# Performance work log

Hardware: AMD Instinct MI355X
Metric: run time of the kernel (lower is better)

Reference implementation:

```python
import jax, jax.numpy as jnp
import numpy as np

B, N, D, NS, HID = 256, 1024, 64, 8, 128
ITERS, SINK_ITERS, MESH_ITERS = 3, 8, 4
MESH_LR = 3.0
EPS = 1e-8


def _grid():
    # build_coords with latent_resolution=(32,32): meshgrid('xy'), flattened to [1024,2]
    x = np.linspace(0.0, 1.0, 32)
    xv, yv = np.meshgrid(x, x)
    g = np.stack([xv.reshape(-1), yv.reshape(-1)], axis=-1)
    return jnp.asarray(g, dtype=jnp.float32)


def layer_norm(x, g, b):
    m = jnp.mean(x, axis=-1, keepdims=True)
    v = jnp.var(x, axis=-1, keepdims=True)
    return (x - m) * jax.lax.rsqrt(v + 1e-5) * g + b


def cdist(k, q):
    # Euclidean pairwise distance: k [b,n,d], q [b,s,d] -> [b,n,s]
    d2 = (jnp.sum(k * k, -1)[..., :, None] + jnp.sum(q * q, -1)[..., None, :]
          - 2.0 * jnp.einsum('bnd,bsd->bns', k, q))
    return jnp.sqrt(jnp.maximum(d2, 1e-12))


def sinkhorn(C, a, b, u=None, v=None, n_iters=SINK_ITERS):
    # log-domain Sinkhorn; C [b,n,s], row marginal a [b,n], col marginal b [b,s]
    log_a = jnp.log(a + EPS)
    log_b = jnp.log(b + EPS)
    if u is None:
        u = jnp.zeros_like(a)
    if v is None:
        v = jnp.zeros_like(b)
    K = -C

    def body(carry, _):
        u, v = carry
        u = log_a - jax.scipy.special.logsumexp(K + v[..., None, :], axis=-1)
        v = log_b - jax.scipy.special.logsumexp(K + u[..., :, None], axis=-2)
        return (u, v), None

    (u, v), _ = jax.lax.scan(body, (u, v), None, length=n_iters)
    P = jnp.exp(K + u[..., :, None] + v[..., None, :])
    return P, u, v


def minimize_entropy_of_sinkhorn(C0, a, b, mesh_lr=MESH_LR, n_mesh_iters=MESH_ITERS):
    # MESH: gradient descent on the cost matrix to minimize Sinkhorn plan entropy
    def ent(C):
        P, u, v = sinkhorn(C, a, b)
        H = -jnp.sum(P * jnp.log(P + EPS))
        return H, (u, v)

    C = C0
    u = v = None
    for _ in range(n_mesh_iters):
        (_, (u, v)), g = jax.value_and_grad(ent, has_aux=True)(C)
        C = C - mesh_lr * g
    return C, u, v


def gru_cell(x, h, w_ih, w_hh, b_ih, b_hh):
    gi = x @ w_ih.T + b_ih
    gh = h @ w_hh.T + b_hh
    i_r, i_z, i_n = jnp.split(gi, 3, axis=-1)
    h_r, h_z, h_n = jnp.split(gh, 3, axis=-1)
    r = jax.nn.sigmoid(i_r + h_r)
    z = jax.nn.sigmoid(i_z + h_z)
    n = jnp.tanh(i_n + r * h_n)
    return (1.0 - z) * n + z * h


def setup_inputs() -> dict:
    key = jax.random.key(0)
    ks = jax.random.split(key, 16)
    s = D ** -0.5
    inp = {
        'inputs': jax.random.normal(ks[0], (B, N, D), jnp.float32),
        'noise': jax.random.normal(ks[1], (B, NS, D), jnp.float32),
        'slots_mu': jax.random.normal(ks[2], (1, 1, D), jnp.float32),
        'slots_sigma': jax.random.uniform(ks[3], (1, 1, D), jnp.float32),
        'Wq': jax.random.normal(ks[4], (D, D), jnp.float32) * s,
        'Wk': jax.random.normal(ks[5], (D, D), jnp.float32) * s,
        'Wv': jax.random.normal(ks[6], (D, D), jnp.float32) * s,
        'gru_w_ih': jax.random.normal(ks[7], (3 * D, D), jnp.float32) * s,
        'gru_w_hh': jax.random.normal(ks[8], (3 * D, D), jnp.float32) * s,
        'gru_b_ih': jnp.zeros((3 * D,), jnp.float32),
        'gru_b_hh': jnp.zeros((3 * D,), jnp.float32),
        'fc1_w': jax.random.normal(ks[9], (HID, D), jnp.float32) * s,
        'fc1_b': jnp.zeros((HID,), jnp.float32),
        'fc2_w': jax.random.normal(ks[10], (D, HID), jnp.float32) * (HID ** -0.5),
        'fc2_b': jnp.zeros((D,), jnp.float32),
        'ln_in_g': jnp.ones((D,), jnp.float32), 'ln_in_b': jnp.zeros((D,), jnp.float32),
        'ln_slots_g': jnp.ones((D,), jnp.float32), 'ln_slots_b': jnp.zeros((D,), jnp.float32),
        'ln_ff_g': jnp.ones((D,), jnp.float32), 'ln_ff_b': jnp.zeros((D,), jnp.float32),
        'wi_w': jax.random.normal(ks[11], (1, D), jnp.float32) * s,
        'wi_b': jnp.zeros((1,), jnp.float32),
        'ws_w': jax.random.normal(ks[12], (1, D), jnp.float32) * s,
        'ws_b': jnp.zeros((1,), jnp.float32),
    }
    return inp


def _forward(inputs, noise, slots_mu, slots_sigma, Wq, Wk, Wv,
             gru_w_ih, gru_w_hh, gru_b_ih, gru_b_hh,
             fc1_w, fc1_b, fc2_w, fc2_b,
             ln_in_g, ln_in_b, ln_slots_g, ln_slots_b, ln_ff_g, ln_ff_b,
             wi_w, wi_b, ws_w, ws_b):
    b_s, n, d = inputs.shape
    n_s = NS
    # slots ~ Normal(mu, |sigma|+eps) via reparameterized noise
    slots = slots_mu + (jnp.abs(slots_sigma) + EPS) * noise  # [b, n_s, d]

    x = layer_norm(inputs, ln_in_g, ln_in_b)
    k = x @ Wk.T
    v = x @ Wv.T
    grid = _grid()  # [N, 2]
    a = jax.nn.softmax((x @ wi_w.T + wi_b)[..., 0], axis=-1) * n_s  # [b, n]

    for _ in range(ITERS):
        slots_prev = slots
        s_n = layer_norm(slots, ln_slots_g, ln_slots_b)
        bm = jax.nn.softmax((s_n @ ws_w.T + ws_b)[..., 0], axis=-1) * n_s  # [b, n_s]
        q = s_n @ Wq.T
        C = cdist(k, q)  # [b, n, n_s]
        C, p, qq = minimize_entropy_of_sinkhorn(C, a, bm)
        attn, _, _ = sinkhorn(C, a, bm, u=p, v=qq)
        attn = jnp.transpose(attn, (0, 2, 1))  # [b, n_s, n]
        updates = attn @ v  # [b, n_s, d]
        slot_pos = jnp.einsum('bqk,kd->bqd', attn, grid)  # [b, n_s, 2]
        slots = gru_cell(updates.reshape(b_s * n_s, d),
                         slots_prev.reshape(b_s * n_s, d),
                         gru_w_ih, gru_w_hh, gru_b_ih, gru_b_hh).reshape(b_s, n_s, d)
        slots = slots + (jax.nn.relu(layer_norm(slots, ln_ff_g, ln_ff_b) @ fc1_w.T + fc1_b) @ fc2_w.T + fc2_b)
    return slots, slot_pos.reshape(b_s, n_s, 2), attn


def reference(inputs, noise, slots_mu, slots_sigma, Wq, Wk, Wv,
              gru_w_ih, gru_w_hh, gru_b_ih, gru_b_hh,
              fc1_w, fc1_b, fc2_w, fc2_b,
              ln_in_g, ln_in_b, ln_slots_g, ln_slots_b, ln_ff_g, ln_ff_b,
              wi_w, wi_b, ws_w, ws_b):
    return _forward(inputs, noise, slots_mu, slots_sigma, Wq, Wk, Wv,
                    gru_w_ih, gru_w_hh, gru_b_ih, gru_b_hh,
                    fc1_w, fc1_b, fc2_w, fc2_b,
                    ln_in_g, ln_in_b, ln_slots_g, ln_slots_b, ln_ff_g, ln_ff_b,
                    wi_w, wi_b, ws_w, ws_b)
```

## Files before the change

kernel.cpp:

```cpp
#include <hip/hip_runtime.h>
#include <math.h>

#define NB   256
#define NN   1024
#define ND   64
#define NSL  8
#define NHID 128
#define N_SINK 8
#define N_MESH 4
#define F_LR  3.0f
#define F_EPS 1e-8f

__global__ __launch_bounds__(256) void k_pre(
    const float* __restrict__ inp, const float* __restrict__ Wk,
    const float* __restrict__ lng, const float* __restrict__ lnb,
    const float* __restrict__ wiw, const float* __restrict__ wib,
    float* __restrict__ xout, float* __restrict__ kkout, float* __restrict__ wilog) {
  __shared__ __align__(16) float xs[4][64];
  int wv = threadIdx.x >> 6, ln = threadIdx.x & 63;
  size_t row = (size_t)blockIdx.x * 4 + wv;
  float xi = inp[row * 64 + ln];
  float s1 = xi, s2 = xi * xi;
  #pragma unroll
  for (int m = 32; m >= 1; m >>= 1) { s1 += __shfl_xor(s1, m, 64); s2 += __shfl_xor(s2, m, 64); }
  float mean = s1 * (1.f / 64.f);
  float var  = s2 * (1.f / 64.f) - mean * mean;
  float xn = (xi - mean) * rsqrtf(var + 1e-5f) * lng[ln] + lnb[ln];
  xs[wv][ln] = xn;
  xout[row * 64 + ln] = xn;
  float wl = xn * wiw[ln];
  #pragma unroll
  for (int m = 32; m >= 1; m >>= 1) wl += __shfl_xor(wl, m, 64);
  __syncthreads();
  const float4* w4 = (const float4*)(Wk + ln * 64);
  const float4* x4 = (const float4*)xs[wv];
  float ko = 0.f;
  #pragma unroll
  for (int c = 0; c < 16; ++c) {
    float4 a = w4[c], xv = x4[c];
    ko += a.x * xv.x + a.y * xv.y + a.z * xv.z + a.w * xv.w;
  }
  float kk = ko * ko;
  #pragma unroll
  for (int m = 32; m >= 1; m >>= 1) kk += __shfl_xor(kk, m, 64);
  if (ln == 0) { kkout[row] = kk; wilog[row] = wl + wib[0]; }
}

__global__ __launch_bounds__(1024) void k_mega(
    const float* __restrict__ noise, const float* __restrict__ mu,
    const float* __restrict__ sigma,
    const float* __restrict__ xg, const float* __restrict__ kkg,
    const float* __restrict__ wilogg,
    const float* __restrict__ Wq, const float* __restrict__ Wk,
    const float* __restrict__ Wv,
    const float* __restrict__ wih, const float* __restrict__ whh,
    const float* __restrict__ bih, const float* __restrict__ bhh,
    const float* __restrict__ fc1w, const float* __restrict__ fc1b,
    const float* __restrict__ fc2w, const float* __restrict__ fc2b,
    const float* __restrict__ lns_g, const float* __restrict__ lns_b,
    const float* __restrict__ lnf_g, const float* __restrict__ lnf_b,
    const float* __restrict__ wsw, const float* __restrict__ wsb,
    float* __restrict__ out_slots, float* __restrict__ out_pos,
    float* __restrict__ out_attn) {
  __shared__ __align__(16) float know[8][NN];
  __shared__ __align__(16) union {
    float uhist[N_SINK][NN];
    float part[16][8][64];
  } U;
  __shared__ __align__(16) float dsb[NN];
  __shared__ __align__(16) float la_lds[NN];
  __shared__ __align__(16) float slot_lds[8][64];
  __shared__ __align__(16) float sn[8][64];
  __shared__ __align__(16) float qsh[8][64];
  __shared__ __align__(16) float qs[8][64];
  __shared__ __align__(16) float updl[8][64];
  __shared__ __align__(16) float ys[8][64];
  __shared__ __align__(16) float rs[8][128];
  __shared__ float vbc[8];
  __shared__ float vbarbc[8];
  __shared__ float vhist[N_SINK][8];
  __shared__ float bmv[8], q2s[8], lbs[8];
  __shared__ float redf[16], bcf[1];

  int b = blockIdx.x, tid = threadIdx.x;
  int wv = tid >> 6, ln = tid & 63;

  if (tid < 512) {
    slot_lds[tid >> 6][ln] = mu[ln] + (fabsf(sigma[ln]) + F_EPS) * noise[(size_t)b * 512 + tid];
  }
  float wl = wilogg[(size_t)b * NN + tid];
  float m0 = wl;
  #pragma unroll
  for (int s = 32; s >= 1; s >>= 1) m0 = fmaxf(m0, __shfl_xor(m0, s, 64));
  if (ln == 0) redf[wv] = m0;
  __syncthreads();
  if (tid == 0) { float a = redf[0]; for (int w = 1; w < 16; ++w) a = fmaxf(a, redf[w]); bcf[0] = a; }
  __syncthreads();
  m0 = bcf[0];
  float e0 = __expf(wl - m0), se0 = e0;
  #pragma unroll
  for (int s = 32; s >= 1; s >>= 1) se0 += __shfl_xor(se0, s, 64);
  __syncthreads();
  if (ln == 0) redf[wv] = se0;
  __syncthreads();
  if (tid == 0) { float a = 0.f; for (int w = 0; w < 16; ++w) a += redf[w]; bcf[0] = a; }
  __syncthreads();
  float la = __logf(8.f * e0 / bcf[0] + F_EPS);
  la_lds[tid] = la;
  float kk = kkg[(size_t)b * NN + tid];
  const float4* xrow4 = (const float4*)(xg + ((size_t)b * NN + tid) * ND);

  float u = 0.f;

  for (int it = 0; it < 3; ++it) {
    if (wv < 8) {
      float x = slot_lds[wv][ln];
      float s1 = x, s2 = x * x;
      #pragma unroll
      for (int m = 32; m >= 1; m >>= 1) { s1 += __shfl_xor(s1, m, 64); s2 += __shfl_xor(s2, m, 64); }
      float mean = s1 * (1.f / 64.f);
      float var  = s2 * (1.f / 64.f) - mean * mean;
      float xn = (x - mean) * rsqrtf(var + 1e-5f) * lns_g[ln] + lns_b[ln];
      sn[wv][ln] = xn;
      float wlg = xn * wsw[ln];
      #pragma unroll
      for (int m = 32; m >= 1; m >>= 1) wlg += __shfl_xor(wlg, m, 64);
      if (ln == 0) bmv[wv] = wlg + wsb[0];
    }
    __syncthreads();
    if (wv < 8) {
      const float4* w4 = (const float4*)(Wq + ln * 64);
      const float4* x4 = (const float4*)sn[wv];
      float q = 0.f;
      #pragma unroll
      for (int c = 0; c < 16; ++c) {
        float4 a = w4[c], xv = x4[c];
        q += a.x * xv.x + a.y * xv.y + a.z * xv.z + a.w * xv.w;
      }
      qsh[wv][ln] = q;
      float q2 = q * q;
      #pragma unroll
      for (int m = 32; m >= 1; m >>= 1) q2 += __shfl_xor(q2, m, 64);
      if (ln == 0) q2s[wv] = q2;
    }
    if (tid >= 512 && tid < 520) {
      int j = tid - 512;
      float mx = bmv[0];
      #pragma unroll
      for (int jj = 1; jj < 8; ++jj) mx = fmaxf(mx, bmv[jj]);
      float ss = 0.f;
      #pragma unroll
      for (int jj = 0; jj < 8; ++jj) ss += __expf(bmv[jj] - mx);
      lbs[j] = __logf(8.f * __expf(bmv[j] - mx) / ss + F_EPS);
    }
    __syncthreads();
    if (wv < 8) {
      float qt = 0.f;
      for (int o = 0; o < 64; ++o) qt = fmaf(qsh[wv][o], Wk[o * 64 + ln], qt);
      qs[wv][ln] = qt;
    }
    __syncthreads();

    {
      float dot[8];
      #pragma unroll
      for (int j = 0; j < 8; ++j) dot[j] = 0.f;
      #pragma unroll 4
      for (int c = 0; c < 16; ++c) {
        float4 xv = xrow4[c];
        #pragma unroll
        for (int j = 0; j < 8; ++j) {
          const float4 qv = *(const float4*)&qs[j][c * 4];
          dot[j] += xv.x * qv.x + xv.y * qv.y + xv.z * qv.z + xv.w * qv.w;
        }
      }
      #pragma unroll
      for (int j = 0; j < 8; ++j) {
        float d2 = kk + q2s[j] - 2.f * dot[j];
        know[j][tid] = -sqrtf(fmaxf(d2, 1e-12f));
      }
    }
    for (int phase = 0; phase <= N_MESH; ++phase) {
      bool cold = (phase < N_MESH);
      for (int t = 0; t < N_SINK; ++t) {
        bool z0 = cold && (t == 0);
        float kv[8];
        #pragma unroll
        for (int j = 0; j < 8; ++j) kv[j] = know[j][tid] + (z0 ? 0.f : vbc[j]);
        float mx = kv[0];
        #pragma unroll
        for (int j = 1; j < 8; ++j) mx = fmaxf(mx, kv[j]);
        float se = 0.f;
        #pragma unroll
        for (int j = 0; j < 8; ++j) se += __expf(kv[j] - mx);
        u = la - (mx + __logf(se));
        U.uhist[t][tid] = u;
        __syncthreads();
        if (wv < 8) {
          float tv[16];
          #pragma unroll
          for (int k = 0; k < 16; ++k) tv[k] = know[wv][ln + k * 64] + U.uhist[t][ln + k * 64];
          float M = tv[0];
          #pragma unroll
          for (int k = 1; k < 16; ++k) M = fmaxf(M, tv[k]);
          #pragma unroll
          for (int d = 32; d >= 1; d >>= 1) M = fmaxf(M, __shfl_xor(M, d, 64));
          float S = 0.f;
          #pragma unroll
          for (int k = 0; k < 16; ++k) S += __expf(tv[k] - M);
          #pragma unroll
          for (int d = 32; d >= 1; d >>= 1) S += __shfl_xor(S, d, 64);
          if (ln == 0) {
            float vj = lbs[wv] - (M + __logf(S));
            vbc[wv] = vj; vhist[t][wv] = vj;
          }
        }
        __syncthreads();
      }
      if (phase == N_MESH) break;

      float Kbar[8], ubarT;
      {
        float gsum = 0.f;
        #pragma unroll
        for (int j = 0; j < 8; ++j) {
          float P  = __expf(know[j][tid] + u + vbc[j]);
          float pe = P + F_EPS;
          float gp = -(__logf(pe) + P / pe) * P;
          Kbar[j] = gp; gsum += gp;
        }
        ubarT = gsum;
      }
      if (wv < 8) {
        float vj = vbc[wv];
        float S = 0.f;
        #pragma unroll
        for (int k = 0; k < 16; ++k) {
          int i = ln + k * 64;
          float P  = __expf(know[wv][i] + U.uhist[N_SINK - 1][i] + vj);
          float pe = P + F_EPS;
          S += -(__logf(pe) + P / pe) * P;
        }
        #pragma unroll
        for (int d = 32; d >= 1; d >>= 1) S += __shfl_xor(S, d, 64);
        if (ln == 0) vbarbc[wv] = S;
      }
      __syncthreads();
      for (int t = N_SINK - 1; t >= 0; --t) {
        float ut = U.uhist[t][tid];
        float dsum = (t == N_SINK - 1) ? ubarT : 0.f;
        #pragma unroll
        for (int j = 0; j < 8; ++j) {
          float w  = __expf(know[j][tid] + ut + vhist[t][j] - lbs[j]);
          float vw = vbarbc[j] * w;
          Kbar[j] -= vw; dsum -= vw;
        }
        #pragma unroll
        for (int j = 0; j < 8; ++j) {
          float vprev = (t > 0) ? vhist[t - 1][j] : 0.f;
          float z  = __expf(know[j][tid] + vprev + ut - la);
          Kbar[j] -= dsum * z;
        }
        if (t > 0) {
          dsb[tid] = dsum;
          __syncthreads();
          if (wv < 8) {
            float vp = vhist[t - 1][wv];
            float S = 0.f;
            #pragma unroll
            for (int k = 0; k < 16; ++k) {
              int i = ln + k * 64;
              float z = __expf(know[wv][i] + vp + U.uhist[t][i] - la_lds[i]);
              S += dsb[i] * z;
            }
            #pragma unroll
            for (int d = 32; d >= 1; d >>= 1) S += __shfl_xor(S, d, 64);
            if (ln == 0) vbarbc[wv] = -S;
          }
          __syncthreads();
        }
      }
      #pragma unroll
      for (int j = 0; j < 8; ++j) know[j][tid] -= F_LR * Kbar[j];
    }
    #pragma unroll
    for (int j = 0; j < 8; ++j) {
      float P = __expf(know[j][tid] + u + vbc[j]);
      know[j][tid] = P;
      if (it == 2) out_attn[((size_t)b * 8 + j) * NN + tid] = P;
    }
    __syncthreads();

    {
      float acc[8];
      #pragma unroll
      for (int j = 0; j < 8; ++j) acc[j] = 0.f;
      const float* xc = xg + ((size_t)b * NN + wv * 64) * ND + ln;
      #pragma unroll 2
      for (int i0 = 0; i0 < 64; i0 += 4) {
        float x0 = xc[(size_t)(i0 + 0) * 64];
        float x1 = xc[(size_t)(i0 + 1) * 64];
        float x2 = xc[(size_t)(i0 + 2) * 64];
        float x3 = xc[(size_t)(i0 + 3) * 64];
        int ir = wv * 64 + i0;
        #pragma unroll
        for (int j = 0; j < 8; ++j) {
          float4 a = *(const float4*)&know[j][ir];
          acc[j] += a.x * x0 + a.y * x1 + a.z * x2 + a.w * x3;
        }
      }
      #pragma unroll
      for (int j = 0; j < 8; ++j) U.part[wv][j][ln] = acc[j];
    }
    if (it == 2 && wv < 8) {
      float px = 0.f, py = 0.f;
      #pragma unroll
      for (int k = 0; k < 16; ++k) {
        int i = ln + k * 64;
        float a = know[wv][i];
        px += a * (float)(i & 31);
        py += a * (float)(i >> 5);
      }
      #pragma unroll
      for (int m = 32; m >= 1; m >>= 1) { px += __shfl_xor(px, m, 64); py += __shfl_xor(py, m, 64); }
      if (ln == 0) {
        out_pos[(b * 8 + wv) * 2 + 0] = px * (1.f / 31.f);
        out_pos[(b * 8 + wv) * 2 + 1] = py * (1.f / 31.f);
      }
    }
    __syncthreads();
    if (wv < 8) {
      float s = 0.f;
      #pragma unroll
      for (int w = 0; w < 16; ++w) s += U.part[w][wv][ln];
      updl[wv][ln] = s;
    }
    __syncthreads();
    if (wv < 8) {
      const float4* w4 = (const float4*)(Wv + ln * 64);
      const float4* u4 = (const float4*)updl[wv];
      float updv = 0.f;
      #pragma unroll
      for (int c = 0; c < 16; ++c) {
        float4 uv = u4[c], wvv = w4[c];
        updv += uv.x * wvv.x + uv.y * wvv.y + uv.z * wvv.z + uv.w * wvv.w;
      }
      sn[wv][ln] = updv;
    }
    __syncthreads();

    float hn = 0.f;
    if (wv < 8) {
      float h = slot_lds[wv][ln];
      float gi0 = bih[ln], gi1 = bih[64 + ln], gi2 = bih[128 + ln];
      float gh0 = bhh[ln], gh1 = bhh[64 + ln], gh2 = bhh[128 + ln];
      const float4* x4 = (const float4*)sn[wv];
      const float4* h4 = (const float4*)slot_lds[wv];
      const float4* wi0 = (const float4*)(wih + (size_t)ln * 64);
      const float4* wi1 = (const float4*)(wih + (size_t)(64 + ln) * 64);
      const float4* wi2 = (const float4*)(wih + (size_t)(128 + ln) * 64);
      const float4* wh0 = (const float4*)(whh + (size_t)ln * 64);
      const float4* wh1 = (const float4*)(whh + (size_t)(64 + ln) * 64);
      const float4* wh2 = (const float4*)(whh + (size_t)(128 + ln) * 64);
      #pragma unroll 2
      for (int c = 0; c < 16; ++c) {
        float4 xv = x4[c], hv = h4[c], a;
        a = wi0[c]; gi0 += xv.x * a.x + xv.y * a.y + xv.z * a.z + xv.w * a.w;
        a = wi1[c]; gi1 += xv.x * a.x + xv.y * a.y + xv.z * a.z + xv.w * a.w;
        a = wi2[c]; gi2 += xv.x * a.x + xv.y * a.y + xv.z * a.z + xv.w * a.w;
        a = wh0[c]; gh0 += hv.x * a.x + hv.y * a.y + hv.z * a.z + hv.w * a.w;
        a = wh1[c]; gh1 += hv.x * a.x + hv.y * a.y + hv.z * a.z + hv.w * a.w;
        a = wh2[c]; gh2 += hv.x * a.x + hv.y * a.y + hv.z * a.z + hv.w * a.w;
      }
      float r = 1.f / (1.f + expf(-(gi0 + gh0)));
      float z = 1.f / (1.f + expf(-(gi1 + gh1)));
      float n = tanhf(gi2 + r * gh2);
      hn = (1.f - z) * n + z * h;
      float s1 = hn, s2 = hn * hn;
      #pragma unroll
      for (int m = 32; m >= 1; m >>= 1) { s1 += __shfl_xor(s1, m, 64); s2 += __shfl_xor(s2, m, 64); }
      float mean = s1 * (1.f / 64.f);
      float var  = s2 * (1.f / 64.f) - mean * mean;
      ys[wv][ln] = (hn - mean) * rsqrtf(var + 1e-5f) * lnf_g[ln] + lnf_b[ln];
    }
    __syncthreads();
    if (wv < 8) {
      float a0 = fc1b[ln], a1 = fc1b[64 + ln];
      const float4* y4 = (const float4*)ys[wv];
      const float4* f0 = (const float4*)(fc1w + (size_t)ln * 64);
      const float4* f1 = (const float4*)(fc1w + (size_t)(64 + ln) * 64);
      #pragma unroll 2
      for (int c = 0; c < 16; ++c) {
        float4 yv = y4[c], a = f0[c], bb = f1[c];
        a0 += yv.x * a.x + yv.y * a.y + yv.z * a.z + yv.w * a.w;
        a1 += yv.x * bb.x + yv.y * bb.y + yv.z * bb.z + yv.w * bb.w;
      }
      rs[wv][ln] = fmaxf(a0, 0.f);
      rs[wv][64 + ln] = fmaxf(a1, 0.f);
    }
    __syncthreads();
    if (wv < 8) {
      float o = fc2b[ln];
      const float4* r4 = (const float4*)rs[wv];
      const float4* f2 = (const float4*)(fc2w + (size_t)ln * 128);
      #pragma unroll 2
      for (int c = 0; c < 32; ++c) {
        float4 rv = r4[c], a = f2[c];
        o += rv.x * a.x + rv.y * a.y + rv.z * a.z + rv.w * a.w;
      }
      slot_lds[wv][ln] = hn + o;
    }
    __syncthreads();
  }
  if (tid < 512) out_slots[(size_t)b * 512 + tid] = slot_lds[tid >> 6][ln];
}

extern "C" void kernel_launch(void* const* d_in, const int* in_sizes, int n_in,
                              void* d_out, int out_size, void* d_ws, size_t ws_size,
                              hipStream_t stream) {
  const float* inputs = (const float*)d_in[0];
  const float* noise  = (const float*)d_in[1];
  const float* mu     = (const float*)d_in[2];
  const float* sigma  = (const float*)d_in[3];
  const float* Wq     = (const float*)d_in[4];
  const float* Wk     = (const float*)d_in[5];
  const float* Wv     = (const float*)d_in[6];
  const float* gwih   = (const float*)d_in[7];
  const float* gwhh   = (const float*)d_in[8];
  const float* gbih   = (const float*)d_in[9];
  const float* gbhh   = (const float*)d_in[10];
  const float* fc1w   = (const float*)d_in[11];
  const float* fc1b   = (const float*)d_in[12];
  const float* fc2w   = (const float*)d_in[13];
  const float* fc2b   = (const float*)d_in[14];
  const float* lnin_g = (const float*)d_in[15];
  const float* lnin_b = (const float*)d_in[16];
  const float* lns_g  = (const float*)d_in[17];
  const float* lns_b  = (const float*)d_in[18];
  const float* lnf_g  = (const float*)d_in[19];
  const float* lnf_b  = (const float*)d_in[20];
  const float* wi_w   = (const float*)d_in[21];
  const float* wi_b   = (const float*)d_in[22];
  const float* ws_w   = (const float*)d_in[23];
  const float* ws_b   = (const float*)d_in[24];

  float* out       = (float*)d_out;
  float* out_slots = out;
  float* out_pos   = out + NB * NSL * ND;
  float* out_attn  = out_pos + NB * NSL * 2;

  float* p = (float*)d_ws;
  float* xbuf  = p; p += (size_t)NB * NN * ND;
  float* kkbuf = p; p += (size_t)NB * NN;
  float* wilog = p; p += (size_t)NB * NN;

  k_pre<<<(NB * NN) / 4, 256, 0, stream>>>(inputs, Wk, lnin_g, lnin_b, wi_w, wi_b,
                                           xbuf, kkbuf, wilog);
  k_mega<<<NB, 1024, 0, stream>>>(noise, mu, sigma, xbuf, kkbuf, wilog,
                                  Wq, Wk, Wv, gwih, gwhh, gbih, gbhh,
                                  fc1w, fc1b, fc2w, fc2b,
                                  lns_g, lns_b, lnf_g, lnf_b, ws_w, ws_b,
                                  out_slots, out_pos, out_attn);
}
```

Measured before the change: 1.317 ms.

## Convert log-domain Sinkhorn and its backward pass to scaling-domain multiplications

Replaces the log-domain Sinkhorn iterations (logsumexp with max and exp per element) by the equivalent scaling form: the kernel stores exp(-C) and uses multiplicative row and column scalings f and g. The hand-written backward pass through the Sinkhorn iterations is rewritten the same way, so most per-element exp and log calls become multiplies. The MESH update becomes a multiplicative exp(-lr*grad) on the kernel matrix. The risk is numerical: without max subtraction, small exp values can underflow or overflow, which changes accuracy relative to the log-domain reference.

```diff
diff --git a/kernel.cpp b/kernel.cpp
--- a/kernel.cpp
+++ b/kernel.cpp
@@ -64,11 +64,10 @@
     float* __restrict__ out_attn) {
   __shared__ __align__(16) float know[8][NN];
   __shared__ __align__(16) union {
-    float uhist[N_SINK][NN];
+    float fhist[N_SINK][NN];
     float part[16][8][64];
   } U;
   __shared__ __align__(16) float dsb[NN];
-  __shared__ __align__(16) float la_lds[NN];
   __shared__ __align__(16) float slot_lds[8][64];
   __shared__ __align__(16) float sn[8][64];
   __shared__ __align__(16) float qsh[8][64];
@@ -76,10 +75,11 @@
   __shared__ __align__(16) float updl[8][64];
   __shared__ __align__(16) float ys[8][64];
   __shared__ __align__(16) float rs[8][128];
-  __shared__ float vbc[8];
+  __shared__ float gbc[8];
   __shared__ float vbarbc[8];
-  __shared__ float vhist[N_SINK][8];
-  __shared__ float bmv[8], q2s[8], lbs[8];
+  __shared__ float ghist[N_SINK][8];
+  __shared__ float gBh[N_SINK][8];
+  __shared__ float bmv[8], q2s[8], Bs[8], rBs[8];
   __shared__ float redf[16], bcf[1];
 
   int b = blockIdx.x, tid = threadIdx.x;
@@ -105,12 +105,10 @@
   __syncthreads();
   if (tid == 0) { float a = 0.f; for (int w = 0; w < 16; ++w) a += redf[w]; bcf[0] = a; }
   __syncthreads();
-  float la = __logf(8.f * e0 / bcf[0] + F_EPS);
-  la_lds[tid] = la;
+  float Ai  = 8.f * e0 / bcf[0] + F_EPS;
+  float rAi = __frcp_rn(Ai);
   float kk = kkg[(size_t)b * NN + tid];
   const float4* xrow4 = (const float4*)(xg + ((size_t)b * NN + tid) * ND);
-
-  float u = 0.f;
 
   for (int it = 0; it < 3; ++it) {
     if (wv < 8) {
@@ -151,7 +149,8 @@
       float ss = 0.f;
       #pragma unroll
       for (int jj = 0; jj < 8; ++jj) ss += __expf(bmv[jj] - mx);
-      lbs[j] = __logf(8.f * __expf(bmv[j] - mx) / ss + F_EPS);
+      float Bj = 8.f * __expf(bmv[j] - mx) / ss + F_EPS;
+      Bs[j] = Bj; rBs[j] = __frcp_rn(Bj);
     }
     __syncthreads();
     if (wv < 8) {
@@ -161,6 +160,7 @@
     }
     __syncthreads();
 
+    float Mreg[8];
     {
       float dot[8];
       #pragma unroll
@@ -177,42 +177,38 @@
       #pragma unroll
       for (int j = 0; j < 8; ++j) {
         float d2 = kk + q2s[j] - 2.f * dot[j];
-        know[j][tid] = -sqrtf(fmaxf(d2, 1e-12f));
-      }
-    }
+        float K = -sqrtf(fmaxf(d2, 1e-12f));
+        Mreg[j] = __expf(K);
+        know[j][tid] = Mreg[j];
+      }
+    }
+    float f = 0.f;
     for (int phase = 0; phase <= N_MESH; ++phase) {
       bool cold = (phase < N_MESH);
       for (int t = 0; t < N_SINK; ++t) {
-        bool z0 = cold && (t == 0);
-        float kv[8];
-        #pragma unroll
-        for (int j = 0; j < 8; ++j) kv[j] = know[j][tid] + (z0 ? 0.f : vbc[j]);
-        float mx = kv[0];
-        #pragma unroll
-        for (int j = 1; j < 8; ++j) mx = fmaxf(mx, kv[j]);
         float se = 0.f;
-        #pragma unroll
-        for (int j = 0; j < 8; ++j) se += __expf(kv[j] - mx);
-        u = la - (mx + __logf(se));
-        U.uhist[t][tid] = u;
+        if (cold && t == 0) {
+          #pragma unroll
+          for (int j = 0; j < 8; ++j) se += Mreg[j];
+        } else {
+          #pragma unroll
+          for (int j = 0; j < 8; ++j) se += Mreg[j] * gbc[j];
+        }
+        f = __fdividef(Ai, se);
+        U.fhist[t][tid] = f;
         __syncthreads();
         if (wv < 8) {
-          float tv[16];
-          #pragma unroll
-          for (int k = 0; k < 16; ++k) tv[k] = know[wv][ln + k * 64] + U.uhist[t][ln + k * 64];
-          float M = tv[0];
-          #pragma unroll
-          for (int k = 1; k < 16; ++k) M = fmaxf(M, tv[k]);
-          #pragma unroll
-          for (int d = 32; d >= 1; d >>= 1) M = fmaxf(M, __shfl_xor(M, d, 64));
           float S = 0.f;
           #pragma unroll
-          for (int k = 0; k < 16; ++k) S += __expf(tv[k] - M);
+          for (int k = 0; k < 16; ++k) {
+            int i = ln + k * 64;
+            S += know[wv][i] * U.fhist[t][i];
+          }
           #pragma unroll
           for (int d = 32; d >= 1; d >>= 1) S += __shfl_xor(S, d, 64);
           if (ln == 0) {
-            float vj = lbs[wv] - (M + __logf(S));
-            vbc[wv] = vj; vhist[t][wv] = vj;
+            float g = __fdividef(Bs[wv], S);
+            gbc[wv] = g; ghist[t][wv] = g; gBh[t][wv] = g * rBs[wv];
           }
         }
         __syncthreads();
@@ -224,22 +220,22 @@
         float gsum = 0.f;
         #pragma unroll
         for (int j = 0; j < 8; ++j) {
-          float P  = __expf(know[j][tid] + u + vbc[j]);
+          float P  = Mreg[j] * f * gbc[j];
           float pe = P + F_EPS;
-          float gp = -(__logf(pe) + P / pe) * P;
+          float gp = -(__logf(pe) + __fdividef(P, pe)) * P;
           Kbar[j] = gp; gsum += gp;
         }
         ubarT = gsum;
       }
       if (wv < 8) {
-        float vj = vbc[wv];
+        float gw = gbc[wv];
         float S = 0.f;
         #pragma unroll
         for (int k = 0; k < 16; ++k) {
           int i = ln + k * 64;
-          float P  = __expf(know[wv][i] + U.uhist[N_SINK - 1][i] + vj);
+          float P  = know[wv][i] * U.fhist[N_SINK - 1][i] * gw;
           float pe = P + F_EPS;
-          S += -(__logf(pe) + P / pe) * P;
+          S += -(__logf(pe) + __fdividef(P, pe)) * P;
         }
         #pragma unroll
         for (int d = 32; d >= 1; d >>= 1) S += __shfl_xor(S, d, 64);
@@ -247,45 +243,45 @@
       }
       __syncthreads();
       for (int t = N_SINK - 1; t >= 0; --t) {
-        float ut = U.uhist[t][tid];
+        float ft = U.fhist[t][tid];
         float dsum = (t == N_SINK - 1) ? ubarT : 0.f;
         #pragma unroll
         for (int j = 0; j < 8; ++j) {
-          float w  = __expf(know[j][tid] + ut + vhist[t][j] - lbs[j]);
-          float vw = vbarbc[j] * w;
+          float vw = vbarbc[j] * gBh[t][j] * (Mreg[j] * ft);
           Kbar[j] -= vw; dsum -= vw;
         }
-        #pragma unroll
-        for (int j = 0; j < 8; ++j) {
-          float vprev = (t > 0) ? vhist[t - 1][j] : 0.f;
-          float z  = __expf(know[j][tid] + vprev + ut - la);
-          Kbar[j] -= dsum * z;
-        }
+        float dfa = dsum * ft * rAi;
         if (t > 0) {
-          dsb[tid] = dsum;
+          #pragma unroll
+          for (int j = 0; j < 8; ++j) Kbar[j] -= dfa * Mreg[j] * ghist[t - 1][j];
+          dsb[tid] = dfa;
           __syncthreads();
           if (wv < 8) {
-            float vp = vhist[t - 1][wv];
             float S = 0.f;
             #pragma unroll
             for (int k = 0; k < 16; ++k) {
               int i = ln + k * 64;
-              float z = __expf(know[wv][i] + vp + U.uhist[t][i] - la_lds[i]);
-              S += dsb[i] * z;
+              S += know[wv][i] * dsb[i];
             }
             #pragma unroll
             for (int d = 32; d >= 1; d >>= 1) S += __shfl_xor(S, d, 64);
-            if (ln == 0) vbarbc[wv] = -S;
+            if (ln == 0) vbarbc[wv] = -ghist[t - 1][wv] * S;
           }
           __syncthreads();
-        }
-      }
-      #pragma unroll
-      for (int j = 0; j < 8; ++j) know[j][tid] -= F_LR * Kbar[j];
+        } else {
+          #pragma unroll
+          for (int j = 0; j < 8; ++j) Kbar[j] -= dfa * Mreg[j];
+        }
+      }
+      #pragma unroll
+      for (int j = 0; j < 8; ++j) {
+        Mreg[j] *= __expf(-F_LR * Kbar[j]);
+        know[j][tid] = Mreg[j];
+      }
     }
     #pragma unroll
     for (int j = 0; j < 8; ++j) {
-      float P = __expf(know[j][tid] + u + vbc[j]);
+      float P = Mreg[j] * f * gbc[j];
       know[j][tid] = P;
       if (it == 2) out_attn[((size_t)b * 8 + j) * NN + tid] = P;
     }
```

Measured after the change: 1.109 ms. -15.8%, faster.
